# Kernel optimization log

Hardware: AMD Instinct MI355X
Metric: run time of the kernel (lower is better)

The kernel has to match this reference:

```python
import jax, jax.numpy as jnp
import numpy as np

ALPHA = 1.0
EPS = 1e-7


def _giou_loss(pred, tgt):
    # pred, tgt: [..., 4] in (x1, y1, x2, y2); returns per-box loss 1 - GIoU
    px1, py1, px2, py2 = pred[..., 0], pred[..., 1], pred[..., 2], pred[..., 3]
    tx1, ty1, tx2, ty2 = tgt[..., 0], tgt[..., 1], tgt[..., 2], tgt[..., 3]
    area_p = (px2 - px1) * (py2 - py1)
    area_t = (tx2 - tx1) * (ty2 - ty1)
    iw = jnp.clip(jnp.minimum(px2, tx2) - jnp.maximum(px1, tx1), 0.0)
    ih = jnp.clip(jnp.minimum(py2, ty2) - jnp.maximum(py1, ty1), 0.0)
    inter = iw * ih
    union = area_p + area_t - inter
    iou = inter / (union + EPS)
    cw = jnp.maximum(px2, tx2) - jnp.minimum(px1, tx1)
    ch = jnp.maximum(py2, ty2) - jnp.minimum(py1, ty1)
    area_c = cw * ch
    giou = iou - (area_c - union) / (area_c + EPS)
    return 1.0 - giou


def _make_boxes(key, shape):
    k1, k2 = jax.random.split(key)
    xy1 = jax.random.uniform(k1, shape + (2,), jnp.float32) * 0.5
    wh = jax.random.uniform(k2, shape + (2,), jnp.float32) * 0.4 + 0.01
    return jnp.concatenate([xy1, xy1 + wh], axis=-1)


def setup_inputs() -> dict:
    key = jax.random.key(0)
    kc, kl, kt, kcls, kp = jax.random.split(key, 5)
    B, A, C = 64, 8732, 81
    confidences = jax.random.normal(kc, (B, A, C), jnp.float32)
    localizations = _make_boxes(kl, (B, A))
    tboxes = _make_boxes(kt, (B, A))
    is_pos = jax.random.uniform(kp, (B, A)) < 0.02
    cls = jnp.where(is_pos, jax.random.randint(kcls, (B, A), 1, C), 0)
    targets = jnp.concatenate([tboxes, cls[..., None].astype(jnp.float32)], axis=-1)
    return {"confidences": confidences, "localizations": localizations, "targets": targets}


def reference(confidences, localizations, targets):
    B, A, C = confidences.shape
    labels = targets[..., 4].astype(jnp.int32)     # [B, A]
    tboxes = targets[..., :4]                      # [B, A, 4]
    pos = labels > 0                               # [B, A]
    nm = pos.sum(axis=-1)                          # [B] num matched per item

    logp = jax.nn.log_softmax(confidences, axis=-1)          # [B, A, C]
    ce = -jnp.take_along_axis(logp, labels[..., None], axis=-1)[..., 0]  # CE vs label
    pos_loss = jnp.where(pos, ce, 0.0).sum(axis=-1)          # [B]

    # hard negative mining: CE vs background (class 0) on negatives only,
    # sort descending, keep top 3 * num_matched. CE >= 0, so mark positives
    # with -1 sentinel; they sort to the end and are excluded by (>= 0).
    neg_ce = jnp.where(pos, -1.0, -logp[..., 0])             # [B, A]
    sneg = -jnp.sort(-neg_ce, axis=-1)                       # descending
    ranks = jnp.arange(A)
    take = (ranks[None, :] < (3 * nm)[:, None]) & (sneg >= 0.0)
    neg_loss = jnp.where(take, sneg, 0.0).sum(axis=-1)       # [B]

    gl = _giou_loss(localizations, tboxes)                   # [B, A]
    loc_loss = jnp.where(pos, gl, 0.0).sum(axis=-1)          # [B]

    num_hits = nm.sum()
    total = (pos_loss + neg_loss + ALPHA * loc_loss).sum()
    denom = jnp.maximum(num_hits, 1).astype(total.dtype)
    has_hits = num_hits > 0
    loss = jnp.where(has_hits, total / denom, 0.0)
    conf_breakdown = jnp.where(has_hits, (pos_loss + neg_loss).sum() / denom, 0.0)
    loc_breakdown = jnp.where(has_hits, loc_loss.sum() / denom, 0.0)
    return loss, conf_breakdown, loc_breakdown
```

## Files before the change

### kernel.cpp

```cpp
#include <hip/hip_runtime.h>
#include <math.h>

#define NCLS 81
#define A_ANCH 8732
#define B_BATCH 64
#define NANCH (B_BATCH * A_ANCH)
#define EPSF 1e-7f

#define TILE 8
#define TDW  (TILE * NCLS)
#define BUFDW 768
#define WPB 8
#define BLK (WPB * 64)
#define GRIDB 768
#define NWAVES (GRIDB * WPB)
#define NT (NANCH / TILE)

static const size_t SBYTES = (size_t)NANCH * sizeof(float);

#define GLOAD_LDS16(g, l) __builtin_amdgcn_global_load_lds( \
    (const __attribute__((address_space(1))) void*)(g),      \
    (__attribute__((address_space(3))) void*)(l), 16, 0, 0)

__device__ __forceinline__ void stage_tile(const float* __restrict__ g,
                                           float* lb, int ln) {
    #pragma unroll
    for (int c = 0; c < 3; ++c) {
        GLOAD_LDS16(g + c * 256 + ln * 4, lb + c * 256);
    }
}

__global__ __launch_bounds__(BLK, 6) void lse_kernel(
    const float* __restrict__ conf, float* __restrict__ sout,
    double* __restrict__ accum, unsigned long long* __restrict__ hits)
{
    __shared__ float sb[WPB][2][BUFDW];

    int tid = threadIdx.x;
    int wv = tid >> 6, ln = tid & 63;
    if (blockIdx.x == 0 && tid == 0) {
        accum[0] = 0.0; accum[1] = 0.0; *hits = 0ull;
    }

    int w = blockIdx.x * WPB + wv;
    int a = ln >> 3, l = ln & 7;

    int t = w;
    stage_tile(conf + (size_t)t * TDW, &sb[wv][0][0], ln);
    int par = 0;

    #pragma clang loop unroll(disable)
    for (; t < NT; t += NWAVES) {
        int tn = t + NWAVES;
        bool more = (tn < NT);
        if (more) stage_tile(conf + (size_t)tn * TDW, &sb[wv][par ^ 1][0], ln);

        if (more) { asm volatile("s_waitcnt vmcnt(3)" ::: "memory"); }
        else      { asm volatile("s_waitcnt vmcnt(0)" ::: "memory"); }
        __builtin_amdgcn_sched_barrier(0);

        const float* r = &sb[wv][par][a * 81 + l * 10];
        float x0 = r[0];
        float e0 = 0.f, e1 = 0.f;
        #pragma unroll
        for (int j = 0; j < 10; j += 2) {
            e0 += __expf(r[j]);
            e1 += __expf(r[j + 1]);
        }
        float s = e0 + e1;
        if (l == 7) s += __expf(r[10]);
        s += __shfl_xor(s, 1);
        s += __shfl_xor(s, 2);
        s += __shfl_xor(s, 4);
        if (l == 0) sout[(size_t)t * TILE + a] = __logf(s) - x0;

        par ^= 1;
    }
}

#define K2_T 1024
#define VPT 9

__global__ __launch_bounds__(K2_T) void mine_kernel(
    const float* __restrict__ conf, const float* __restrict__ loc,
    const float* __restrict__ tgt, const float* __restrict__ sout,
    double* __restrict__ accum, unsigned long long* __restrict__ hits)
{
    __shared__ int   cnt[34];
    __shared__ float fs[4];
    __shared__ int   nm_s;
    int b = blockIdx.x, tid = threadIdx.x, lane = tid & 63;
    if (tid < 34) cnt[tid] = 0;
    if (tid < 4)  fs[tid] = 0.f;
    if (tid == 0) nm_s = 0;
    __syncthreads();

    float v[VPT]; int lab[VPT];
    size_t base = (size_t)b * A_ANCH;
    #pragma unroll
    for (int i = 0; i < VPT; ++i) {
        int idx = tid + i * K2_T;
        bool in = idx < A_ANCH;
        v[i]   = in ? sout[base + idx] : -1.f;
        lab[i] = in ? (int)tgt[(base + idx) * 5 + 4] : 0;
    }

    float pce = 0.f, ploc = 0.f; int pc = 0;
    #pragma unroll
    for (int i = 0; i < VPT; ++i) {
        if (lab[i] > 0) {
            size_t gi = base + (size_t)(tid + i * K2_T);
            float r0 = conf[gi * NCLS];
            float rl = conf[gi * NCLS + lab[i]];
            pce += v[i] + r0 - rl;
            float4 p = *(const float4*)(loc + gi * 4);
            const float* tg = tgt + gi * 5;
            float tx1 = tg[0], ty1 = tg[1], tx2 = tg[2], ty2 = tg[3];
            float area_p = (p.z - p.x) * (p.w - p.y);
            float area_t = (tx2 - tx1) * (ty2 - ty1);
            float iw = fmaxf(fminf(p.z, tx2) - fmaxf(p.x, tx1), 0.f);
            float ih = fmaxf(fminf(p.w, ty2) - fmaxf(p.y, ty1), 0.f);
            float inter = iw * ih;
            float uni   = area_p + area_t - inter;
            float iou   = inter / (uni + EPSF);
            float cw = fmaxf(p.z, tx2) - fminf(p.x, tx1);
            float ch = fmaxf(p.w, ty2) - fminf(p.y, ty1);
            float area_c = cw * ch;
            ploc += 1.f - (iou - (area_c - uni) / (area_c + EPSF));
            pc++;
            v[i] = -1.f;
        }
    }
    for (int off = 32; off; off >>= 1) {
        pc   += __shfl_xor(pc, off);
        pce  += __shfl_xor(pce, off);
        ploc += __shfl_xor(ploc, off);
    }
    if (lane == 0) {
        if (pc) atomicAdd(&nm_s, pc);
        atomicAdd(&fs[2], pce);
        atomicAdd(&fs[3], ploc);
    }

    int c = 0; float sa = 0.f;
    #pragma unroll
    for (int i = 0; i < VPT; ++i) { if (v[i] >= 0.f) { c++; sa += v[i]; } }
    for (int off = 32; off; off >>= 1) { c += __shfl_xor(c, off); sa += __shfl_xor(sa, off); }
    if (lane == 0) { atomicAdd(&cnt[32], c); atomicAdd(&fs[0], sa); }
    __syncthreads();

    int k = 3 * nm_s;
    int c0 = cnt[32]; float sall = fs[0];
    float negl = 0.f;
    if (k >= c0) {
        negl = sall;
    } else if (k > 0) {
        unsigned lo = 0u, hi = 0x7F800000u;
        int it = 0;
        while (hi - lo > 1u) {
            unsigned mid = lo + (hi - lo) / 2u;
            float thr = __uint_as_float(mid);
            int cc = 0;
            #pragma unroll
            for (int i = 0; i < VPT; ++i) cc += (v[i] >= thr) ? 1 : 0;
            for (int off = 32; off; off >>= 1) cc += __shfl_xor(cc, off);
            if (lane == 0) atomicAdd(&cnt[it], cc);
            __syncthreads();
            if (cnt[it] >= k) lo = mid; else hi = mid;
            ++it;
        }
        float tth = __uint_as_float(lo);
        int cg = 0; float sg = 0.f;
        #pragma unroll
        for (int i = 0; i < VPT; ++i) { if (v[i] > tth) { cg++; sg += v[i]; } }
        for (int off = 32; off; off >>= 1) { cg += __shfl_xor(cg, off); sg += __shfl_xor(sg, off); }
        if (lane == 0) { atomicAdd(&cnt[33], cg); atomicAdd(&fs[1], sg); }
        __syncthreads();
        negl = fs[1] + (float)(k - cnt[33]) * tth;
    }

    if (tid == 0) {
        atomicAdd(&accum[0], (double)(fs[2] + negl));
        atomicAdd(&accum[1], (double)fs[3]);
        atomicAdd(hits, (unsigned long long)nm_s);
    }
}

__global__ void finalize_kernel(const double* __restrict__ accum,
                                const unsigned long long* __restrict__ hits,
                                float* __restrict__ out) {
    if (threadIdx.x == 0 && blockIdx.x == 0) {
        double conf_s = accum[0], loc_s = accum[1];
        unsigned long long h = *hits;
        double denom = (double)(h > 0 ? h : 1ull);
        if (h > 0) {
            out[0] = (float)((conf_s + loc_s) / denom);
            out[1] = (float)(conf_s / denom);
            out[2] = (float)(loc_s / denom);
        } else {
            out[0] = 0.f; out[1] = 0.f; out[2] = 0.f;
        }
    }
}

extern "C" void kernel_launch(void* const* d_in, const int* in_sizes, int n_in,
                              void* d_out, int out_size, void* d_ws, size_t ws_size,
                              hipStream_t stream) {
    const float* conf = (const float*)d_in[0];
    const float* loc  = (const float*)d_in[1];
    const float* tgt  = (const float*)d_in[2];
    float* out = (float*)d_out;

    char* ws = (char*)d_ws;
    float* sout = (float*)ws;
    double* accum = (double*)(ws + SBYTES);
    unsigned long long* hits = (unsigned long long*)(ws + SBYTES + 16);

    lse_kernel<<<dim3(GRIDB), dim3(BLK), 0, stream>>>(conf, sout, accum, hits);
    mine_kernel<<<dim3(B_BATCH), dim3(K2_T), 0, stream>>>(
        conf, loc, tgt, sout, accum, hits);
    finalize_kernel<<<1, 64, 0, stream>>>(accum, hits, out);
}
```

Measured before the change: 62.62 us.

## Fuse LSE, mining and finalize into one persistent kernel with grid barrier

Merges the three launches into a single kernel. Each wave now processes a contiguous run of tiles, and the first 64 blocks handle positive-anchor CE and GIoU work before a global atomic counter barrier, then do hard-negative mining. The last block to finish computes the final outputs. The point is to remove launch gaps and overlap positive-anchor work with the LSE pass. The cost is a spin-wait grid barrier that assumes all 768 blocks are co-resident, plus an extra memset launch.

```diff
diff --git a/kernel.cpp b/kernel.cpp
--- a/kernel.cpp
+++ b/kernel.cpp
@@ -15,6 +15,10 @@
 #define GRIDB 768
 #define NWAVES (GRIDB * WPB)
 #define NT (NANCH / TILE)
+#define MW 512
+#define QM 9
+
+#define VPT 18
 
 static const size_t SBYTES = (size_t)NANCH * sizeof(float);
 
@@ -30,30 +34,40 @@
     }
 }
 
-__global__ __launch_bounds__(BLK, 6) void lse_kernel(
-    const float* __restrict__ conf, float* __restrict__ sout,
-    double* __restrict__ accum, unsigned long long* __restrict__ hits)
+__device__ __forceinline__ void wave_run(int w, int& S, int& E) {
+    int s, q;
+    if (w < MW)            { q = 9;  s = 9 * w; }
+    else if (w < MW + 3296){ q = 12; s = 4608 + 12 * (w - MW); }
+    else                   { q = 11; s = 44160 + 11 * (w - MW - 3296); }
+    S = s; E = s + q;
+}
+
+__global__ __launch_bounds__(BLK, 6) void ssd_fused_kernel(
+    const float* __restrict__ conf, const float* __restrict__ loc,
+    const float* __restrict__ tgt, float* __restrict__ sout,
+    double* __restrict__ accum, unsigned long long* __restrict__ hits,
+    unsigned int* __restrict__ ctr, unsigned int* __restrict__ ctr2,
+    float* __restrict__ out)
 {
     __shared__ float sb[WPB][2][BUFDW];
+    __shared__ int   cnt[34];
+    __shared__ float fs[4];
+    __shared__ int   nm_s;
 
     int tid = threadIdx.x;
     int wv = tid >> 6, ln = tid & 63;
-    if (blockIdx.x == 0 && tid == 0) {
-        accum[0] = 0.0; accum[1] = 0.0; *hits = 0ull;
-    }
-
-    int w = blockIdx.x * WPB + wv;
+    int bid = blockIdx.x;
+    int w = bid * WPB + wv;
     int a = ln >> 3, l = ln & 7;
 
-    int t = w;
-    stage_tile(conf + (size_t)t * TDW, &sb[wv][0][0], ln);
+    int S, E; wave_run(w, S, E);
+    stage_tile(conf + (size_t)S * TDW, &sb[wv][0][0], ln);
     int par = 0;
 
     #pragma clang loop unroll(disable)
-    for (; t < NT; t += NWAVES) {
-        int tn = t + NWAVES;
-        bool more = (tn < NT);
-        if (more) stage_tile(conf + (size_t)tn * TDW, &sb[wv][par ^ 1][0], ln);
+    for (int t = S; t < E; ++t) {
+        bool more = (t + 1 < E);
+        if (more) stage_tile(conf + (size_t)(t + 1) * TDW, &sb[wv][par ^ 1][0], ln);
 
         if (more) { asm volatile("s_waitcnt vmcnt(3)" ::: "memory"); }
         else      { asm volatile("s_waitcnt vmcnt(0)" ::: "memory"); }
@@ -76,77 +90,86 @@
 
         par ^= 1;
     }
-}
-
-#define K2_T 1024
-#define VPT 9
-
-__global__ __launch_bounds__(K2_T) void mine_kernel(
-    const float* __restrict__ conf, const float* __restrict__ loc,
-    const float* __restrict__ tgt, const float* __restrict__ sout,
-    double* __restrict__ accum, unsigned long long* __restrict__ hits)
-{
-    __shared__ int   cnt[34];
-    __shared__ float fs[4];
-    __shared__ int   nm_s;
-    int b = blockIdx.x, tid = threadIdx.x, lane = tid & 63;
-    if (tid < 34) cnt[tid] = 0;
-    if (tid < 4)  fs[tid] = 0.f;
-    if (tid == 0) nm_s = 0;
+
+    bool miner = (bid < B_BATCH);
+    size_t base = (size_t)bid * A_ANCH;
+    unsigned posmask = 0u;
+    float corr = 0.f, ploc = 0.f; int pc = 0;
+
+    if (miner) {
+        if (tid < 34) cnt[tid] = 0;
+        if (tid < 4)  fs[tid] = 0.f;
+        if (tid == 0) nm_s = 0;
+        #pragma unroll
+        for (int i = 0; i < VPT; ++i) {
+            int idx = tid + i * BLK;
+            int lab = (idx < A_ANCH) ? (int)tgt[(base + idx) * 5 + 4] : 0;
+            if (lab > 0) {
+                posmask |= (1u << i);
+                size_t gi = base + idx;
+                corr += conf[gi * NCLS] - conf[gi * NCLS + lab];
+                float4 p = *(const float4*)(loc + gi * 4);
+                const float* tg = tgt + gi * 5;
+                float tx1 = tg[0], ty1 = tg[1], tx2 = tg[2], ty2 = tg[3];
+                float area_p = (p.z - p.x) * (p.w - p.y);
+                float area_t = (tx2 - tx1) * (ty2 - ty1);
+                float iw = fmaxf(fminf(p.z, tx2) - fmaxf(p.x, tx1), 0.f);
+                float ih = fmaxf(fminf(p.w, ty2) - fmaxf(p.y, ty1), 0.f);
+                float inter = iw * ih;
+                float uni   = area_p + area_t - inter;
+                float iou   = inter / (uni + EPSF);
+                float cw = fmaxf(p.z, tx2) - fminf(p.x, tx1);
+                float ch = fmaxf(p.w, ty2) - fminf(p.y, ty1);
+                float area_c = cw * ch;
+                ploc += 1.f - (iou - (area_c - uni) / (area_c + EPSF));
+                pc++;
+            }
+        }
+        int lane = tid & 63;
+        float lcorr = corr, lploc = ploc; int lpc = pc;
+        for (int off = 32; off; off >>= 1) {
+            lpc   += __shfl_xor(lpc, off);
+            lcorr += __shfl_xor(lcorr, off);
+            lploc += __shfl_xor(lploc, off);
+        }
+        __syncthreads();
+        if (lane == 0) {
+            if (lpc) atomicAdd(&nm_s, lpc);
+            atomicAdd(&fs[2], lcorr);
+            atomicAdd(&fs[3], lploc);
+        }
+    }
+
     __syncthreads();
-
-    float v[VPT]; int lab[VPT];
-    size_t base = (size_t)b * A_ANCH;
+    if (tid == 0) {
+        __threadfence();
+        __hip_atomic_fetch_add(ctr, 1u, __ATOMIC_ACQ_REL, __HIP_MEMORY_SCOPE_AGENT);
+    }
+    if (!miner) return;
+    if (tid == 0) {
+        while (__hip_atomic_load(ctr, __ATOMIC_ACQUIRE, __HIP_MEMORY_SCOPE_AGENT) < GRIDB) {
+            __builtin_amdgcn_s_sleep(1);
+        }
+    }
+    __syncthreads();
+
+    float v[VPT];
+    float pce_v = 0.f;
     #pragma unroll
     for (int i = 0; i < VPT; ++i) {
-        int idx = tid + i * K2_T;
-        bool in = idx < A_ANCH;
-        v[i]   = in ? sout[base + idx] : -1.f;
-        lab[i] = in ? (int)tgt[(base + idx) * 5 + 4] : 0;
-    }
-
-    float pce = 0.f, ploc = 0.f; int pc = 0;
-    #pragma unroll
-    for (int i = 0; i < VPT; ++i) {
-        if (lab[i] > 0) {
-            size_t gi = base + (size_t)(tid + i * K2_T);
-            float r0 = conf[gi * NCLS];
-            float rl = conf[gi * NCLS + lab[i]];
-            pce += v[i] + r0 - rl;
-            float4 p = *(const float4*)(loc + gi * 4);
-            const float* tg = tgt + gi * 5;
-            float tx1 = tg[0], ty1 = tg[1], tx2 = tg[2], ty2 = tg[3];
-            float area_p = (p.z - p.x) * (p.w - p.y);
-            float area_t = (tx2 - tx1) * (ty2 - ty1);
-            float iw = fmaxf(fminf(p.z, tx2) - fmaxf(p.x, tx1), 0.f);
-            float ih = fmaxf(fminf(p.w, ty2) - fmaxf(p.y, ty1), 0.f);
-            float inter = iw * ih;
-            float uni   = area_p + area_t - inter;
-            float iou   = inter / (uni + EPSF);
-            float cw = fmaxf(p.z, tx2) - fminf(p.x, tx1);
-            float ch = fmaxf(p.w, ty2) - fminf(p.y, ty1);
-            float area_c = cw * ch;
-            ploc += 1.f - (iou - (area_c - uni) / (area_c + EPSF));
-            pc++;
-            v[i] = -1.f;
-        }
-    }
-    for (int off = 32; off; off >>= 1) {
-        pc   += __shfl_xor(pc, off);
-        pce  += __shfl_xor(pce, off);
-        ploc += __shfl_xor(ploc, off);
-    }
-    if (lane == 0) {
-        if (pc) atomicAdd(&nm_s, pc);
-        atomicAdd(&fs[2], pce);
-        atomicAdd(&fs[3], ploc);
-    }
-
+        int idx = tid + i * BLK;
+        v[i] = (idx < A_ANCH) ? sout[base + idx] : -1.f;
+        if (posmask & (1u << i)) { pce_v += v[i]; v[i] = -1.f; }
+    }
+    int lane = tid & 63;
     int c = 0; float sa = 0.f;
     #pragma unroll
     for (int i = 0; i < VPT; ++i) { if (v[i] >= 0.f) { c++; sa += v[i]; } }
-    for (int off = 32; off; off >>= 1) { c += __shfl_xor(c, off); sa += __shfl_xor(sa, off); }
-    if (lane == 0) { atomicAdd(&cnt[32], c); atomicAdd(&fs[0], sa); }
+    float lpce = pce_v;
+    for (int off = 32; off; off >>= 1) {
+        c += __shfl_xor(c, off); sa += __shfl_xor(sa, off); lpce += __shfl_xor(lpce, off);
+    }
+    if (lane == 0) { atomicAdd(&cnt[32], c); atomicAdd(&fs[0], sa); atomicAdd(&fs[2], lpce); }
     __syncthreads();
 
     int k = 3 * nm_s;
@@ -183,22 +206,20 @@
         atomicAdd(&accum[0], (double)(fs[2] + negl));
         atomicAdd(&accum[1], (double)fs[3]);
         atomicAdd(hits, (unsigned long long)nm_s);
-    }
-}
-
-__global__ void finalize_kernel(const double* __restrict__ accum,
-                                const unsigned long long* __restrict__ hits,
-                                float* __restrict__ out) {
-    if (threadIdx.x == 0 && blockIdx.x == 0) {
-        double conf_s = accum[0], loc_s = accum[1];
-        unsigned long long h = *hits;
-        double denom = (double)(h > 0 ? h : 1ull);
-        if (h > 0) {
-            out[0] = (float)((conf_s + loc_s) / denom);
-            out[1] = (float)(conf_s / denom);
-            out[2] = (float)(loc_s / denom);
-        } else {
-            out[0] = 0.f; out[1] = 0.f; out[2] = 0.f;
+        __threadfence();
+        unsigned old = __hip_atomic_fetch_add(ctr2, 1u, __ATOMIC_ACQ_REL, __HIP_MEMORY_SCOPE_AGENT);
+        if (old == B_BATCH - 1) {
+            double conf_s = __hip_atomic_load(&accum[0], __ATOMIC_ACQUIRE, __HIP_MEMORY_SCOPE_AGENT);
+            double loc_s  = __hip_atomic_load(&accum[1], __ATOMIC_ACQUIRE, __HIP_MEMORY_SCOPE_AGENT);
+            unsigned long long h = __hip_atomic_load(hits, __ATOMIC_ACQUIRE, __HIP_MEMORY_SCOPE_AGENT);
+            double denom = (double)(h > 0 ? h : 1ull);
+            if (h > 0) {
+                out[0] = (float)((conf_s + loc_s) / denom);
+                out[1] = (float)(conf_s / denom);
+                out[2] = (float)(loc_s / denom);
+            } else {
+                out[0] = 0.f; out[1] = 0.f; out[2] = 0.f;
+            }
         }
     }
 }
@@ -215,9 +236,11 @@
     float* sout = (float*)ws;
     double* accum = (double*)(ws + SBYTES);
     unsigned long long* hits = (unsigned long long*)(ws + SBYTES + 16);
-
-    lse_kernel<<<dim3(GRIDB), dim3(BLK), 0, stream>>>(conf, sout, accum, hits);
-    mine_kernel<<<dim3(B_BATCH), dim3(K2_T), 0, stream>>>(
-        conf, loc, tgt, sout, accum, hits);
-    finalize_kernel<<<1, 64, 0, stream>>>(accum, hits, out);
-}
+    unsigned int* ctr  = (unsigned int*)(ws + SBYTES + 32);
+    unsigned int* ctr2 = (unsigned int*)(ws + SBYTES + 36);
+
+    hipMemsetAsync(ws + SBYTES, 0, 64, stream);
+
+    ssd_fused_kernel<<<dim3(GRIDB), dim3(BLK), 0, stream>>>(
+        conf, loc, tgt, sout, accum, hits, ctr, ctr2, out);
+}
```

Measured after the change: 107.3 us. +71.4%, slower.
